# Kernel tuning notes

Measured on AMD Instinct MI355X. Metric: run time of the kernel, lower is better.

## Reference

```python
import jax, jax.numpy as jnp
import numpy as np

EMBED_DIM = 768
NUM_HEADS = 12
LN_EPS = 1e-5


def _apply_rope3d(p16, e):
    """3-axis RoPE. p16: [B,1,L,3] float16 coords; e: [B,H,L,D] float32.
    Heads split into 3 groups (x/y/z); within each group last dim split in halves
    and rotated by angle coord*freqs (computed in fp16, matching the .half() cast)."""
    B, H, L, D = e.shape
    half = D // 2
    freqs = (10000.0 ** (-jnp.arange(half, dtype=jnp.float32) / half)).astype(jnp.float16)
    ang = p16[..., None] * freqs                     # [B,1,L,3,half] fp16
    ang = jnp.transpose(ang, (0, 3, 1, 2, 4))        # [B,3,1,L,half]
    c, s = jnp.cos(ang), jnp.sin(ang)                # fp16
    eg = e.reshape(B, 3, H // 3, L, D)               # 3 head groups
    e1, e2 = eg[..., :half], eg[..., half:]
    o1 = e1 * c - e2 * s                             # fp16*fp32 -> fp32
    o2 = e2 * c + e1 * s
    return jnp.concatenate([o1, o2], axis=-1).reshape(B, H, L, D)


def setup_inputs() -> dict:
    key = jax.random.key(0)
    ks = jax.random.split(key, 5)
    B, L, C = 4, 2048, EMBED_DIM
    feat = jax.random.normal(ks[0], (B, L, C), dtype=jnp.float32)
    pos = jax.random.normal(ks[1], (B, L, 3), dtype=jnp.float32)
    w_qkv = jax.random.normal(ks[2], (C, 3 * C), dtype=jnp.float32) * (1.0 / np.sqrt(C))
    b_qkv = jnp.zeros((3 * C,), dtype=jnp.float32)
    w_proj = jax.random.normal(ks[3], (C, C), dtype=jnp.float32) * (1.0 / np.sqrt(C))
    b_proj = jnp.zeros((C,), dtype=jnp.float32)
    ln_g = jnp.ones((C,), dtype=jnp.float32)
    ln_b = jnp.zeros((C,), dtype=jnp.float32)
    return {"feat": feat, "pos": pos, "ln_g": ln_g, "ln_b": ln_b,
            "w_qkv": w_qkv, "b_qkv": b_qkv, "w_proj": w_proj, "b_proj": b_proj}


def reference(feat, pos, ln_g, ln_b, w_qkv, b_qkv, w_proj, b_proj):
    B, L, C = feat.shape
    H = NUM_HEADS
    D = C // H
    # LayerNorm
    mu = jnp.mean(feat, axis=-1, keepdims=True)
    var = jnp.mean(jnp.square(feat - mu), axis=-1, keepdims=True)
    x = (feat - mu) * jax.lax.rsqrt(var + LN_EPS) * ln_g + ln_b
    # QKV projection and head split
    qkv = x @ w_qkv + b_qkv
    q, k, v = jnp.split(qkv, 3, axis=-1)
    q = q.reshape(B, L, H, D).transpose(0, 2, 1, 3)  # [B,H,L,D]
    k = k.reshape(B, L, H, D).transpose(0, 2, 1, 3)
    v = v.reshape(B, L, H, D).transpose(0, 2, 1, 3)
    # 3D-coordinate RoPE (angles in fp16 per original .half() cast)
    p16 = pos.astype(jnp.float16)[:, None]           # [B,1,L,3]
    q = _apply_rope3d(p16, q)
    k = _apply_rope3d(p16, k)
    # flex_attention with block_mask=None -> full softmax attention, scale 1/sqrt(D)
    scale = 1.0 / np.sqrt(D)
    att = jax.nn.softmax(jnp.einsum('bhqd,bhkd->bhqk', q, k) * scale, axis=-1)
    out = jnp.einsum('bhqk,bhkd->bhqd', att, v)
    out = out.transpose(0, 2, 1, 3).reshape(B, L, C)
    # output projection (dropout = identity in eval)
    return out @ w_proj + b_proj
```

## Files before the change

### kernel.cpp

```cpp
#include <hip/hip_runtime.h>

typedef unsigned short u16;
typedef unsigned int u32;
typedef __attribute__((ext_vector_type(8))) __bf16 bf16x8;
typedef __attribute__((ext_vector_type(4))) __bf16 bf16x4;
typedef __attribute__((ext_vector_type(8))) u16 ushort8;
typedef __attribute__((ext_vector_type(4))) float f32x4;

#define DEV static __device__ __forceinline__

DEV float bf2f(u16 v) { union { u32 u; float f; } x; x.u = ((u32)v) << 16; return x.f; }
DEV u16 f2bf(float f) {
  u32 u = __builtin_bit_cast(u32, f);
  return (u16)((u + 0x7fffu + ((u >> 16) & 1u)) >> 16);
}
DEV float rnd_bf(float f) { return bf2f(f2bf(f)); }
DEV u32 pack2(float a, float b) { return (u32)f2bf(a) | ((u32)f2bf(b) << 16); }

DEV void gload_lds16(const void* g, void* l) {
  __builtin_amdgcn_global_load_lds((const __attribute__((address_space(1))) u32*)g,
                                   (__attribute__((address_space(3))) u32*)l, 16, 0, 0);
}

DEV f32x4 MFMA16(bf16x8 a, bf16x8 b, f32x4 c) {
  return __builtin_amdgcn_mfma_f32_16x16x32_bf16(a, b, c, 0, 0, 0);
}

#define QSCALE (0.125f * 1.442695040888963f)

__global__ __launch_bounds__(256) void prep_kernel(const float* __restrict__ pos, float2* __restrict__ tab,
                                                   const float* __restrict__ w_qkv, u16* __restrict__ wqkvT,
                                                   const float* __restrict__ w_proj, u16* __restrict__ wprojT,
                                                   const float* __restrict__ feat, const float* __restrict__ gam,
                                                   const float* __restrict__ bet, u16* __restrict__ xo) {
  __shared__ u16 t[64][65];
  const int tid = threadIdx.x;
  const int blk = blockIdx.x;

  if (blk < 3072) {
    int gid = blk * 256 + tid;
    int row = gid & 8191;
    int ad = gid >> 13;
    int axis = ad >> 5, d = ad & 31;
    float p = pos[(size_t)row * 3 + axis];
    float fr = exp2f((float)d * -0.41524101186092029f);
    _Float16 ah = (_Float16)p * (_Float16)fr;
    float sn, cs;
    sincosf((float)ah, &sn, &cs);
    tab[gid] = make_float2((float)(_Float16)cs, (float)(_Float16)sn);
  } else if (blk < 3648) {
    const float* W;
    u16* Wt;
    int rows = 768, cols, bx, by;
    if (blk < 3504) {
      int i2 = blk - 3072;
      W = w_qkv; Wt = wqkvT; cols = 2304; bx = i2 % 36; by = i2 / 36;
    } else {
      int i2 = blk - 3504;
      W = w_proj; Wt = wprojT; cols = 768; bx = i2 % 12; by = i2 / 12;
    }
    const int tr = by << 6, tc = bx << 6;
    {
      int r = tid >> 2, c0 = (tid & 3) << 4;
      const float* src = W + (size_t)(tr + r) * cols + tc + c0;
#pragma unroll
      for (int i = 0; i < 16; i += 4) {
        float4 v = *(const float4*)(src + i);
        t[r][c0 + i]     = f2bf(v.x);
        t[r][c0 + i + 1] = f2bf(v.y);
        t[r][c0 + i + 2] = f2bf(v.z);
        t[r][c0 + i + 3] = f2bf(v.w);
      }
    }
    __syncthreads();
    {
      int dd = tid >> 2, l0 = (tid & 3) << 4;
      ushort8 o0, o1;
#pragma unroll
      for (int i = 0; i < 8; ++i) { o0[i] = t[l0 + i][dd]; o1[i] = t[l0 + 8 + i][dd]; }
      u16* dst = Wt + (size_t)(tc + dd) * rows + tr + l0;
      *(ushort8*)dst = o0;
      *(ushort8*)(dst + 8) = o1;
    }
  } else {
    const int row = (blk - 3648) * 4 + (tid >> 6);
    const int lane = tid & 63;
    const float* f = feat + (size_t)row * 768 + lane * 4;
    float4 v0 = *(const float4*)f;
    float4 v1 = *(const float4*)(f + 256);
    float4 v2 = *(const float4*)(f + 512);
    float s = v0.x + v0.y + v0.z + v0.w + v1.x + v1.y + v1.z + v1.w + v2.x + v2.y + v2.z + v2.w;
    float s2 = v0.x*v0.x + v0.y*v0.y + v0.z*v0.z + v0.w*v0.w
             + v1.x*v1.x + v1.y*v1.y + v1.z*v1.z + v1.w*v1.w
             + v2.x*v2.x + v2.y*v2.y + v2.z*v2.z + v2.w*v2.w;
#pragma unroll
    for (int off = 32; off > 0; off >>= 1) { s += __shfl_xor(s, off); s2 += __shfl_xor(s2, off); }
    const float mu = s * (1.0f / 768.0f);
    const float rstd = rsqrtf(s2 * (1.0f / 768.0f) - mu * mu + 1e-5f);
    u16* o = xo + (size_t)row * 768 + lane * 4;
    const float4* gp = (const float4*)(gam + lane * 4);
    const float4* bp = (const float4*)(bet + lane * 4);
    float4 vv[3] = {v0, v1, v2};
#pragma unroll
    for (int jj = 0; jj < 3; ++jj) {
      float4 gg = gp[jj * 64];
      float4 bb = bp[jj * 64];
      uint2 pk;
      pk.x = pack2((vv[jj].x - mu) * rstd * gg.x + bb.x, (vv[jj].y - mu) * rstd * gg.y + bb.y);
      pk.y = pack2((vv[jj].z - mu) * rstd * gg.z + bb.z, (vv[jj].w - mu) * rstd * gg.w + bb.w);
      *(uint2*)(o + jj * 256) = pk;
    }
  }
}

template<bool ROPE, bool F32OUT>
__global__ __launch_bounds__(256) void gemm_bt(const u16* __restrict__ A, const u16* __restrict__ Bt,
                                               const float* __restrict__ bias, void* __restrict__ Cout,
                                               u16* __restrict__ Qb, u16* __restrict__ Kb,
                                               const float2* __restrict__ tab, int M, int N, int K) {
  __shared__ u16 lds[16384];
  const int tid = threadIdx.x;
  const int lane = tid & 63, wv = tid >> 6;
  const int l16 = lane & 15, g = lane >> 4;
  const int nt = N >> 7;
  int bid = (int)blockIdx.x;
  { const int cpx = (int)gridDim.x >> 3; bid = (bid & 7) * cpx + (bid >> 3); }
  const int bm = bid / nt, bn = bid % nt;
  const int m0 = bm << 7, n0 = bn << 7;
  const int wr = (wv >> 1) << 6, wc = (wv & 1) << 6;
  const int rl = wv * 8 + (lane >> 3);
  const int slot = lane & 7;

  f32x4 acc[4][4] = {};

  for (int k0 = 0; k0 < K; k0 += 64) {
    __syncthreads();
#pragma unroll
    for (int it = 0; it < 4; ++it) {
      int r = it * 32 + rl;
      gload_lds16(A + (size_t)(m0 + r) * K + k0 + 8 * (slot ^ (r & 7)),
                  (char*)lds + it * 4096 + wv * 1024);
      gload_lds16(Bt + (size_t)(n0 + r) * K + k0 + 8 * (slot ^ (r & 7)),
                  (char*)lds + 16384 + it * 4096 + wv * 1024);
    }
    __syncthreads();
#pragma unroll
    for (int ks = 0; ks < 2; ++ks) {
      bf16x8 af[4], bfr[4];
#pragma unroll
      for (int mf = 0; mf < 4; ++mf) {
        int r = wr + mf * 16 + l16;
        af[mf] = *(const bf16x8*)((const char*)lds + r * 128 + ((ks * 64 + g * 16) ^ ((r & 7) << 4)));
      }
#pragma unroll
      for (int nf = 0; nf < 4; ++nf) {
        int r = wc + nf * 16 + l16;
        bfr[nf] = *(const bf16x8*)((const char*)lds + 16384 + r * 128 + ((ks * 64 + g * 16) ^ ((r & 7) << 4)));
      }
#pragma unroll
      for (int mf = 0; mf < 4; ++mf)
#pragma unroll
        for (int nf = 0; nf < 4; ++nf)
          acc[mf][nf] = MFMA16(af[mf], bfr[nf], acc[mf][nf]);
    }
  }

  if (ROPE && n0 < 1536) {
    const int colbase = n0 + wc;
    const bool isQ = colbase < 768;
    const int h = (isQ ? colbase : colbase - 768) >> 6;
    const int axis = h >> 2;
    u16* P = isQ ? Qb : Kb;
#pragma unroll
    for (int nf = 0; nf < 2; ++nf) {
      const int col = n0 + wc + nf * 16 + l16;
      const int d = nf * 16 + l16;
      const float2* trow = tab + (size_t)(axis * 32 + d) * 8192;
      const float b1 = bias[col], b2 = bias[col + 32];
#pragma unroll
      for (int mf = 0; mf < 4; ++mf) {
        int row0 = m0 + wr + mf * 16 + g * 4;
#pragma unroll
        for (int j = 0; j < 4; ++j) {
          int row = row0 + j;
          float2 cs2 = trow[row];
          float c = cs2.x, s = cs2.y;
          float a = acc[mf][nf][j] + b1;
          float bb = acc[mf][nf + 2][j] + b2;
          float o1 = a * c - bb * s;
          float o2 = bb * c + a * s;
          if (isQ) { o1 *= QSCALE; o2 *= QSCALE; }
          size_t obase = ((size_t)((row >> 11) * 12 + h) * 2048 + (row & 2047)) * 64;
          P[obase + d]      = f2bf(o1);
          P[obase + d + 32] = f2bf(o2);
        }
      }
    }
  } else {
    const int colsub = (ROPE ? 1536 : 0);
    const int Nout = (ROPE ? 768 : N);
#pragma unroll
    for (int nf = 0; nf < 4; ++nf) {
      int col = n0 + wc + nf * 16 + l16;
      float bb = bias[col];
#pragma unroll
      for (int mf = 0; mf < 4; ++mf) {
        int row = m0 + wr + mf * 16 + g * 4;
#pragma unroll
        for (int j = 0; j < 4; ++j) {
          float v = acc[mf][nf][j] + bb;
          if (F32OUT) ((float*)Cout)[(size_t)(row + j) * Nout + col - colsub] = rnd_bf(v);
          else        ((u16*)Cout)[(size_t)(row + j) * Nout + col - colsub] = f2bf(v);
        }
      }
    }
  }
}

__global__ __launch_bounds__(256) void v_transpose(const u16* __restrict__ Vp, u16* __restrict__ Vt) {
  __shared__ u16 t[64][65];
  const int tid = threadIdx.x;
  const int lt = blockIdx.x, bh = blockIdx.y;
  const int b = bh / 12, h = bh - b * 12;
  {
    int r = tid >> 2, c0 = (tid & 3) << 4;
    const u16* src = Vp + (size_t)(b * 2048 + lt * 64 + r) * 768 + h * 64 + c0;
    ushort8 a0 = *(const ushort8*)src;
    ushort8 a1 = *(const ushort8*)(src + 8);
#pragma unroll
    for (int i = 0; i < 8; ++i) { t[r][c0 + i] = a0[i]; t[r][c0 + 8 + i] = a1[i]; }
  }
  __syncthreads();
  {
    int dd = tid >> 2, l0 = (tid & 3) << 4;
    ushort8 o0, o1;
#pragma unroll
    for (int i = 0; i < 8; ++i) { o0[i] = t[l0 + i][dd]; o1[i] = t[l0 + 8 + i][dd]; }
    u16* dst = Vt + (size_t)(bh * 64 + dd) * 2048 + lt * 64 + l0;
    *(ushort8*)dst = o0;
    *(ushort8*)(dst + 8) = o1;
  }
}

__global__ __launch_bounds__(256) void attn_kernel(const u16* __restrict__ Q, const u16* __restrict__ K,
                                                   const u16* __restrict__ Vt, u16* __restrict__ O) {
  __shared__ u16 kv_lds[2][8192];
  const int tid = threadIdx.x;
  const int lane = tid & 63, wv = tid >> 6;
  const int l16 = lane & 15, g = lane >> 4;
  int bid = (int)blockIdx.x;
  bid = (bid & 7) * 96 + (bid >> 3);
  const int bh = bid >> 4;
  const int q0 = (bid & 15) * 128 + wv * 32;
  const size_t base = (size_t)bh * (2048 * 64);
  const size_t vbase = (size_t)bh * (64 * 2048);
  const int rl = wv * 8 + (lane >> 3);
  const int slot = lane & 7;

  bf16x8 qf[2][2];
#pragma unroll
  for (int qm = 0; qm < 2; ++qm)
#pragma unroll
    for (int ks = 0; ks < 2; ++ks)
      qf[qm][ks] = *(const bf16x8*)(Q + base + (size_t)(q0 + qm * 16 + l16) * 64 + ks * 32 + g * 8);

  float lsum[2] = {0.f, 0.f};
  f32x4 oacc[2][4] = {};

#pragma unroll
  for (int it = 0; it < 2; ++it) {
    int r = it * 32 + rl;
    gload_lds16(K + base + (size_t)r * 64 + 8 * (slot ^ (r & 7)),
                (char*)kv_lds + it * 4096 + wv * 1024);
    gload_lds16(Vt + vbase + (size_t)r * 2048 + 8 * (slot ^ (r & 7)),
                (char*)kv_lds + 8192 + it * 4096 + wv * 1024);
  }
  __syncthreads();

  int cur = 0;
  for (int kv0 = 0; kv0 < 2048; kv0 += 64) {
    if (kv0 + 64 < 2048) {
#pragma unroll
      for (int it = 0; it < 2; ++it) {
        int r = it * 32 + rl;
        gload_lds16(K + base + (size_t)(kv0 + 64 + r) * 64 + 8 * (slot ^ (r & 7)),
                    (char*)kv_lds + (cur ^ 1) * 16384 + it * 4096 + wv * 1024);
        gload_lds16(Vt + vbase + (size_t)r * 2048 + kv0 + 64 + 8 * (slot ^ (r & 7)),
                    (char*)kv_lds + (cur ^ 1) * 16384 + 8192 + it * 4096 + wv * 1024);
      }
    }

    const char* kb = (const char*)kv_lds + cur * 16384;
    const char* vbuf = kb + 8192;

    f32x4 st[2][4] = {};
#pragma unroll
    for (int ks = 0; ks < 2; ++ks) {
      bf16x8 kf[4];
#pragma unroll
      for (int n = 0; n < 4; ++n) {
        int r = n * 16 + l16;
        kf[n] = *(const bf16x8*)(kb + r * 128 + ((ks * 64 + g * 16) ^ ((r & 7) << 4)));
      }
      __builtin_amdgcn_s_setprio(1);
#pragma unroll
      for (int qm = 0; qm < 2; ++qm)
#pragma unroll
        for (int n = 0; n < 4; ++n)
          st[qm][n] = MFMA16(kf[n], qf[qm][ks], st[qm][n]);
      __builtin_amdgcn_s_setprio(0);
    }

#pragma unroll
    for (int ks2 = 0; ks2 < 2; ++ks2) {
      bf16x8 vf[4];
#pragma unroll
      for (int db = 0; db < 4; ++db) {
        int r = db * 16 + l16;
        int swz = (r & 7) << 4;
        const char* rowb = vbuf + r * 128;
        bf16x4 lo = *(const bf16x4*)(rowb + ((ks2 * 64 + g * 8) ^ swz));
        bf16x4 hi = *(const bf16x4*)(rowb + ((ks2 * 64 + g * 8 + 32) ^ swz));
        vf[db] = __builtin_shufflevector(lo, hi, 0, 1, 2, 3, 4, 5, 6, 7);
      }
      bf16x8 pf[2];
#pragma unroll
      for (int qm = 0; qm < 2; ++qm) {
        float e[8];
#pragma unroll
        for (int j = 0; j < 4; ++j) {
          e[j]     = __builtin_amdgcn_exp2f(st[qm][2 * ks2][j]);
          e[4 + j] = __builtin_amdgcn_exp2f(st[qm][2 * ks2 + 1][j]);
        }
        lsum[qm] += ((e[0] + e[1]) + (e[2] + e[3])) + ((e[4] + e[5]) + (e[6] + e[7]));
        bf16x8 pv;
#pragma unroll
        for (int j = 0; j < 8; ++j) pv[j] = (__bf16)e[j];
        pf[qm] = pv;
      }
      __builtin_amdgcn_s_setprio(1);
#pragma unroll
      for (int qm = 0; qm < 2; ++qm)
#pragma unroll
        for (int db = 0; db < 4; ++db)
          oacc[qm][db] = MFMA16(vf[db], pf[qm], oacc[qm][db]);
      __builtin_amdgcn_s_setprio(0);
    }

    __syncthreads();
    cur ^= 1;
  }

  const int b = bh / 12, h = bh - b * 12;
#pragma unroll
  for (int qm = 0; qm < 2; ++qm) {
    float tot = lsum[qm];
    tot += __shfl_xor(tot, 16);
    tot += __shfl_xor(tot, 32);
    float inv = 1.0f / tot;
    size_t row = (size_t)b * 2048 + q0 + qm * 16 + l16;
#pragma unroll
    for (int db = 0; db < 4; ++db) {
      uint2 pk;
      pk.x = pack2(oacc[qm][db][0] * inv, oacc[qm][db][1] * inv);
      pk.y = pack2(oacc[qm][db][2] * inv, oacc[qm][db][3] * inv);
      *(uint2*)(O + row * 768 + h * 64 + db * 16 + g * 4) = pk;
    }
  }
}

extern "C" void kernel_launch(void* const* d_in, const int* in_sizes, int n_in,
                              void* d_out, int out_size, void* d_ws, size_t ws_size,
                              hipStream_t stream) {
  (void)in_sizes; (void)n_in; (void)out_size; (void)ws_size;
  const float* feat   = (const float*)d_in[0];
  const float* pos    = (const float*)d_in[1];
  const float* ln_g   = (const float*)d_in[2];
  const float* ln_b   = (const float*)d_in[3];
  const float* w_qkv  = (const float*)d_in[4];
  const float* b_qkv  = (const float*)d_in[5];
  const float* w_proj = (const float*)d_in[6];
  const float* b_proj = (const float*)d_in[7];
  float* out = (float*)d_out;
  char* ws = (char*)d_ws;
  u16* xln    = (u16*)(ws);
  u16* wqkvT  = (u16*)(ws + 12582912);
  u16* wprojT = (u16*)(ws + 16121856);
  u16* Qb     = (u16*)(ws + 17301504);
  u16* Kb     = (u16*)(ws + 29884416);
  u16* Vp     = (u16*)(ws + 42467328);
  u16* Vtb    = (u16*)(ws + 55050240);
  u16* attnout= (u16*)(ws + 67633152);
  float2* tab = (float2*)(ws + 80216064);

  prep_kernel<<<5696, 256, 0, stream>>>(pos, tab, w_qkv, wqkvT, w_proj, wprojT, feat, ln_g, ln_b, xln);
  gemm_bt<true, false><<<1152, 256, 0, stream>>>(xln, wqkvT, b_qkv, Vp, Qb, Kb, tab, 8192, 2304, 768);
  v_transpose<<<dim3(32, 48), 256, 0, stream>>>(Vp, Vtb);
  attn_kernel<<<768, 256, 0, stream>>>(Qb, Kb, Vtb, attnout);
  gemm_bt<false, true><<<384, 256, 0, stream>>>(attnout, wprojT, b_proj, out, nullptr, nullptr, nullptr, 8192, 768, 768);
}
```

Before: 155.0 us.

## Triple-buffer attention K/V loads and use 64-row tiles for output projection

The attention kernel moves from double to triple buffering of K/V tiles in LDS. It prefetches two tiles ahead and replaces the full __syncthreads with explicit vmcnt waits plus a barrier, so global loads overlap more with compute. The GEMM gains an M-tile template parameter. The output projection now uses 64-row tiles and twice as many blocks (768) to fill more CUs. In exchange, attention LDS use grows by half, which may lower occupancy, and the hand-counted vmcnt values must match the number of outstanding loads.

Result: slower. 163.4 us (+5.4%).

```diff
diff --git a/kernel.cpp b/kernel.cpp
--- a/kernel.cpp
+++ b/kernel.cpp
@@ -113,12 +113,13 @@
   }
 }
 
-template<bool ROPE, bool F32OUT>
+template<bool ROPE, bool F32OUT, int TM>
 __global__ __launch_bounds__(256) void gemm_bt(const u16* __restrict__ A, const u16* __restrict__ Bt,
                                                const float* __restrict__ bias, void* __restrict__ Cout,
                                                u16* __restrict__ Qb, u16* __restrict__ Kb,
                                                const float2* __restrict__ tab, int M, int N, int K) {
-  __shared__ u16 lds[16384];
+  __shared__ u16 lds[TM * 64 + 8192];
+  constexpr int MF = TM / 32;
   const int tid = threadIdx.x;
   const int lane = tid & 63, wv = tid >> 6;
   const int l16 = lane & 15, g = lane >> 4;
@@ -126,73 +127,81 @@
   int bid = (int)blockIdx.x;
   { const int cpx = (int)gridDim.x >> 3; bid = (bid & 7) * cpx + (bid >> 3); }
   const int bm = bid / nt, bn = bid % nt;
-  const int m0 = bm << 7, n0 = bn << 7;
-  const int wr = (wv >> 1) << 6, wc = (wv & 1) << 6;
+  const int m0 = bm * TM, n0 = bn << 7;
+  const int wr = (wv >> 1) * (TM / 2), wc = (wv & 1) << 6;
   const int rl = wv * 8 + (lane >> 3);
   const int slot = lane & 7;
 
-  f32x4 acc[4][4] = {};
+  f32x4 acc[MF][4] = {};
 
   for (int k0 = 0; k0 < K; k0 += 64) {
     __syncthreads();
 #pragma unroll
-    for (int it = 0; it < 4; ++it) {
+    for (int it = 0; it < TM / 32; ++it) {
       int r = it * 32 + rl;
       gload_lds16(A + (size_t)(m0 + r) * K + k0 + 8 * (slot ^ (r & 7)),
                   (char*)lds + it * 4096 + wv * 1024);
+    }
+#pragma unroll
+    for (int it = 0; it < 4; ++it) {
+      int r = it * 32 + rl;
       gload_lds16(Bt + (size_t)(n0 + r) * K + k0 + 8 * (slot ^ (r & 7)),
-                  (char*)lds + 16384 + it * 4096 + wv * 1024);
+                  (char*)lds + TM * 128 + it * 4096 + wv * 1024);
     }
     __syncthreads();
 #pragma unroll
     for (int ks = 0; ks < 2; ++ks) {
-      bf16x8 af[4], bfr[4];
-#pragma unroll
-      for (int mf = 0; mf < 4; ++mf) {
+      bf16x8 af[MF], bfr[4];
+#pragma unroll
+      for (int mf = 0; mf < MF; ++mf) {
         int r = wr + mf * 16 + l16;
         af[mf] = *(const bf16x8*)((const char*)lds + r * 128 + ((ks * 64 + g * 16) ^ ((r & 7) << 4)));
       }
 #pragma unroll
       for (int nf = 0; nf < 4; ++nf) {
         int r = wc + nf * 16 + l16;
-        bfr[nf] = *(const bf16x8*)((const char*)lds + 16384 + r * 128 + ((ks * 64 + g * 16) ^ ((r & 7) << 4)));
-      }
-#pragma unroll
-      for (int mf = 0; mf < 4; ++mf)
+        bfr[nf] = *(const bf16x8*)((const char*)lds + TM * 128 + r * 128 + ((ks * 64 + g * 16) ^ ((r & 7) << 4)));
+      }
+#pragma unroll
+      for (int mf = 0; mf < MF; ++mf)
 #pragma unroll
         for (int nf = 0; nf < 4; ++nf)
           acc[mf][nf] = MFMA16(af[mf], bfr[nf], acc[mf][nf]);
     }
   }
 
-  if (ROPE && n0 < 1536) {
-    const int colbase = n0 + wc;
-    const bool isQ = colbase < 768;
-    const int h = (isQ ? colbase : colbase - 768) >> 6;
-    const int axis = h >> 2;
-    u16* P = isQ ? Qb : Kb;
-#pragma unroll
-    for (int nf = 0; nf < 2; ++nf) {
-      const int col = n0 + wc + nf * 16 + l16;
-      const int d = nf * 16 + l16;
-      const float2* trow = tab + (size_t)(axis * 32 + d) * 8192;
-      const float b1 = bias[col], b2 = bias[col + 32];
-#pragma unroll
-      for (int mf = 0; mf < 4; ++mf) {
-        int row0 = m0 + wr + mf * 16 + g * 4;
-#pragma unroll
-        for (int j = 0; j < 4; ++j) {
-          int row = row0 + j;
-          float2 cs2 = trow[row];
-          float c = cs2.x, s = cs2.y;
-          float a = acc[mf][nf][j] + b1;
-          float bb = acc[mf][nf + 2][j] + b2;
-          float o1 = a * c - bb * s;
-          float o2 = bb * c + a * s;
-          if (isQ) { o1 *= QSCALE; o2 *= QSCALE; }
-          size_t obase = ((size_t)((row >> 11) * 12 + h) * 2048 + (row & 2047)) * 64;
-          P[obase + d]      = f2bf(o1);
-          P[obase + d + 32] = f2bf(o2);
+  bool ropePath = false;
+  if constexpr (ROPE) ropePath = (n0 < 1536);
+  if (ropePath) {
+    if constexpr (ROPE) {
+      const int colbase = n0 + wc;
+      const bool isQ = colbase < 768;
+      const int h = (isQ ? colbase : colbase - 768) >> 6;
+      const int axis = h >> 2;
+      u16* P = isQ ? Qb : Kb;
+#pragma unroll
+      for (int nf = 0; nf < 2; ++nf) {
+        const int col = n0 + wc + nf * 16 + l16;
+        const int d = nf * 16 + l16;
+        const float2* trow = tab + (size_t)(axis * 32 + d) * 8192;
+        const float b1 = bias[col], b2 = bias[col + 32];
+#pragma unroll
+        for (int mf = 0; mf < MF; ++mf) {
+          int row0 = m0 + wr + mf * 16 + g * 4;
+#pragma unroll
+          for (int j = 0; j < 4; ++j) {
+            int row = row0 + j;
+            float2 cs2 = trow[row];
+            float c = cs2.x, s = cs2.y;
+            float a = acc[mf][nf][j] + b1;
+            float bb = acc[mf][nf + 2][j] + b2;
+            float o1 = a * c - bb * s;
+            float o2 = bb * c + a * s;
+            if (isQ) { o1 *= QSCALE; o2 *= QSCALE; }
+            size_t obase = ((size_t)((row >> 11) * 12 + h) * 2048 + (row & 2047)) * 64;
+            P[obase + d]      = f2bf(o1);
+            P[obase + d + 32] = f2bf(o2);
+          }
         }
       }
     }
@@ -204,7 +213,7 @@
       int col = n0 + wc + nf * 16 + l16;
       float bb = bias[col];
 #pragma unroll
-      for (int mf = 0; mf < 4; ++mf) {
+      for (int mf = 0; mf < MF; ++mf) {
         int row = m0 + wr + mf * 16 + g * 4;
 #pragma unroll
         for (int j = 0; j < 4; ++j) {
@@ -244,7 +253,7 @@
 
 __global__ __launch_bounds__(256) void attn_kernel(const u16* __restrict__ Q, const u16* __restrict__ K,
                                                    const u16* __restrict__ Vt, u16* __restrict__ O) {
-  __shared__ u16 kv_lds[2][8192];
+  __shared__ u16 kv_lds[3][8192];
   const int tid = threadIdx.x;
   const int lane = tid & 63, wv = tid >> 6;
   const int l16 = lane & 15, g = lane >> 4;
@@ -267,30 +276,26 @@
   float lsum[2] = {0.f, 0.f};
   f32x4 oacc[2][4] = {};
 
-#pragma unroll
-  for (int it = 0; it < 2; ++it) {
-    int r = it * 32 + rl;
-    gload_lds16(K + base + (size_t)r * 64 + 8 * (slot ^ (r & 7)),
-                (char*)kv_lds + it * 4096 + wv * 1024);
-    gload_lds16(Vt + vbase + (size_t)r * 2048 + 8 * (slot ^ (r & 7)),
-                (char*)kv_lds + 8192 + it * 4096 + wv * 1024);
-  }
-  __syncthreads();
-
-  int cur = 0;
-  for (int kv0 = 0; kv0 < 2048; kv0 += 64) {
-    if (kv0 + 64 < 2048) {
-#pragma unroll
-      for (int it = 0; it < 2; ++it) {
-        int r = it * 32 + rl;
-        gload_lds16(K + base + (size_t)(kv0 + 64 + r) * 64 + 8 * (slot ^ (r & 7)),
-                    (char*)kv_lds + (cur ^ 1) * 16384 + it * 4096 + wv * 1024);
-        gload_lds16(Vt + vbase + (size_t)r * 2048 + kv0 + 64 + 8 * (slot ^ (r & 7)),
-                    (char*)kv_lds + (cur ^ 1) * 16384 + 8192 + it * 4096 + wv * 1024);
-      }
-    }
-
-    const char* kb = (const char*)kv_lds + cur * 16384;
+  auto STAGE = [&](int tile, int buf) {
+#pragma unroll
+    for (int it = 0; it < 2; ++it) {
+      int r = it * 32 + rl;
+      gload_lds16(K + base + (size_t)(tile * 64 + r) * 64 + 8 * (slot ^ (r & 7)),
+                  (char*)kv_lds + buf * 16384 + it * 4096 + wv * 1024);
+      gload_lds16(Vt + vbase + (size_t)r * 2048 + tile * 64 + 8 * (slot ^ (r & 7)),
+                  (char*)kv_lds + buf * 16384 + 8192 + it * 4096 + wv * 1024);
+    }
+  };
+
+  STAGE(0, 0);
+  STAGE(1, 1);
+  asm volatile("s_waitcnt vmcnt(4)" ::: "memory");
+  __builtin_amdgcn_s_barrier();
+
+  for (int t = 0; t < 32; ++t) {
+    if (t < 30) STAGE(t + 2, (t + 2) % 3);
+
+    const char* kb = (const char*)kv_lds + (t % 3) * 16384;
     const char* vbuf = kb + 8192;
 
     f32x4 st[2][4] = {};
@@ -347,8 +352,11 @@
       __builtin_amdgcn_s_setprio(0);
     }
 
-    __syncthreads();
-    cur ^= 1;
+    if (t < 31) {
+      if (t < 30) asm volatile("s_waitcnt vmcnt(4)" ::: "memory");
+      else        asm volatile("s_waitcnt vmcnt(0)" ::: "memory");
+      __builtin_amdgcn_s_barrier();
+    }
   }
 
   const int b = bh / 12, h = bh - b * 12;
@@ -394,8 +402,8 @@
   float2* tab = (float2*)(ws + 80216064);
 
   prep_kernel<<<5696, 256, 0, stream>>>(pos, tab, w_qkv, wqkvT, w_proj, wprojT, feat, ln_g, ln_b, xln);
-  gemm_bt<true, false><<<1152, 256, 0, stream>>>(xln, wqkvT, b_qkv, Vp, Qb, Kb, tab, 8192, 2304, 768);
+  gemm_bt<true, false, 128><<<1152, 256, 0, stream>>>(xln, wqkvT, b_qkv, Vp, Qb, Kb, tab, 8192, 2304, 768);
   v_transpose<<<dim3(32, 48), 256, 0, stream>>>(Vp, Vtb);
   attn_kernel<<<768, 256, 0, stream>>>(Qb, Kb, Vtb, attnout);
-  gemm_bt<false, true><<<384, 256, 0, stream>>>(attnout, wprojT, b_proj, out, nullptr, nullptr, nullptr, 8192, 768, 768);
-}
+  gemm_bt<false, true, 64><<<768, 256, 0, stream>>>(attnout, wprojT, b_proj, out, nullptr, nullptr, nullptr, 8192, 768, 768);
+}
```
